# Optimization experiments

Measured on AMD Instinct MI355X. Metric: run time of the kernel, lower is better.

Reference implementation:

```python
import jax, jax.numpy as jnp
import numpy as np

N, X_DIM, Y_DIM, HID = 8192, 512, 2048 // 4, 2048
Y_DIM = 512

def setup_inputs() -> dict:
    key = jax.random.key(0)
    ks = jax.random.split(key, 10)
    def lin(k, fan_in, fan_out):
        lim = 1.0 / np.sqrt(fan_in)
        kw, kb = jax.random.split(k)
        W = jax.random.uniform(kw, (fan_in, fan_out), jnp.float32, -lim, lim)
        b = jax.random.uniform(kb, (fan_out,), jnp.float32, -lim, lim)
        return W, b
    mu_W1, mu_b1 = lin(ks[0], X_DIM, HID)
    mu_W2, mu_b2 = lin(ks[1], HID, Y_DIM)
    lv_W1, lv_b1 = lin(ks[2], X_DIM, HID)
    lv_W2, lv_b2 = lin(ks[3], HID, Y_DIM)
    return {
        "x_samples": jax.random.normal(ks[4], (N, X_DIM), jnp.float32),
        "y_samples": jax.random.normal(ks[5], (N, Y_DIM), jnp.float32),
        "mu_W1": mu_W1, "mu_b1": mu_b1, "mu_W2": mu_W2, "mu_b2": mu_b2,
        "lv_W1": lv_W1, "lv_b1": lv_b1, "lv_W2": lv_W2, "lv_b2": lv_b2,
    }

def reference(x_samples, y_samples, mu_W1, mu_b1, mu_W2, mu_b2, lv_W1, lv_b1, lv_W2, lv_b2):
    # MLP heads (GEMMs)
    mu = jax.nn.relu(x_samples @ mu_W1 + mu_b1) @ mu_W2 + mu_b2          # [N, D]
    logvar = jnp.tanh(jax.nn.relu(x_samples @ lv_W1 + lv_b1) @ lv_W2 + lv_b2)  # [N, D]
    w = 0.5 * jnp.exp(-logvar)                                           # 1/(2*exp(logvar))
    n = x_samples.shape[0]

    # positive: -mean_i sum_d (mu_id - y_id)^2 * w_id
    positive = -(((mu - y_samples) ** 2) * w).sum(axis=1).mean()

    # negative (exact decomposition of the [N,N,D] broadcast):
    # -(1/N^2) sum_{i,d} w_id * (N*mu_id^2 - 2*mu_id*Sy_d + Sy2_d)
    Sy = y_samples.sum(axis=0)          # [D]
    Sy2 = (y_samples ** 2).sum(axis=0)  # [D]
    negative = -(w * (n * mu ** 2 - 2.0 * mu * Sy + Sy2)).sum() / (n * n)

    return positive - negative
```

## Files before the change

kernel.cpp:

```cpp
#include <hip/hip_runtime.h>
#include <hip/hip_bf16.h>
#include <stdint.h>

#define NS   8192
#define XD   512
#define HD   2048
#define YD   512

typedef unsigned short u16;
using bf16x8 = __attribute__((ext_vector_type(8))) short;
using f32x4  = __attribute__((ext_vector_type(4))) float;

__device__ __forceinline__ float bf2f(u16 u) {
  union { uint32_t i; float f; } v; v.i = ((uint32_t)u) << 16; return v.f;
}
__device__ __forceinline__ u16 f2b(float f) {
  __hip_bfloat16 hb = __float2bfloat16(f);
  return *(const u16*)&hb;
}
__device__ __forceinline__ float ld_in(const void* p, int f32, size_t i) {
  return f32 ? ((const float*)p)[i] : bf2f(((const u16*)p)[i]);
}
#define GLDS(gp, lp) __builtin_amdgcn_global_load_lds( \
    (__attribute__((address_space(1))) void*)(gp),     \
    (__attribute__((address_space(3))) void*)(lp), 16, 0, 0)

__device__ __forceinline__ int probe_f32(const void* p, int n_u16, int* sflag) {
  if (threadIdx.x == 0) *sflag = 0;
  __syncthreads();
  const u16* q = (const u16*)p;
  int wild = 0;
  for (int i = threadIdx.x; i < n_u16; i += blockDim.x) {
    float v = bf2f(q[i]);
    if (!(fabsf(v) <= 1000.0f)) wild = 1;
  }
  if (wild) *sflag = 1;
  __syncthreads();
  int r = *sflag;
  __syncthreads();
  return r;
}

__global__ __launch_bounds__(256) void prep_all(
    const void* __restrict__ x,
    const void* w1m, const void* b1m, const void* w2m, const void* b2m,
    const void* w1l, const void* b1l, const void* w2l, const void* b2l,
    u16* __restrict__ xb, float* __restrict__ biasv,
    u16* __restrict__ W1t, u16* __restrict__ W2tm, u16* __restrict__ W2tl) {
  __shared__ u16 tile[64 * 72];
  __shared__ int sflag;
  const int b = blockIdx.x;
  const int tid = threadIdx.x;

  if (b < 2048) {
    if (!probe_f32(x, 1024, &sflag)) return;
    const size_t base = (size_t)b * 2048 + (size_t)tid * 8;
    alignas(16) u16 o[8];
    const float4* s = (const float4*)((const float*)x + base);
    float4 v0 = s[0], v1 = s[1];
    o[0]=f2b(v0.x); o[1]=f2b(v0.y); o[2]=f2b(v0.z); o[3]=f2b(v0.w);
    o[4]=f2b(v1.x); o[5]=f2b(v1.y); o[6]=f2b(v1.z); o[7]=f2b(v1.w);
    *(uint4*)(xb + base) = *(const uint4*)o;
  } else if (b == 2048) {
    const int f3 = probe_f32(b1m, 1024, &sflag);
    const int f5 = probe_f32(b2m, 512, &sflag);
    const int f7 = probe_f32(b1l, 1024, &sflag);
    const int f9 = probe_f32(b2l, 512, &sflag);
    for (int i = tid; i < 5120; i += 256) {
      float v;
      if (i < 2048)      v = ld_in(b1m, f3, i);
      else if (i < 4096) v = ld_in(b1l, f7, i - 2048);
      else if (i < 4608) v = ld_in(b2m, f5, i - 4096);
      else               v = ld_in(b2l, f9, i - 4608);
      biasv[i] = v;
    }
  } else {
    const int id = b - 2049, which = id >> 8, t = id & 255;
    const void* in; u16* out; int R, C;
    if (which == 0)      { in = w1m; out = W1t;                   R = XD; C = HD; }
    else if (which == 1) { in = w2m; out = W2tm;                  R = HD; C = YD; }
    else if (which == 2) { in = w1l; out = W1t + (size_t)HD * XD; R = XD; C = HD; }
    else                 { in = w2l; out = W2tl;                  R = HD; C = YD; }
    const int f = probe_f32(in, 1024, &sflag);
    const int nbx = C >> 6;
    const int c0 = (t % nbx) * 64, r0 = (t / nbx) * 64;
    const int r = tid >> 2, cc = (tid & 3) * 16;
    if (f) {
      const float4* s = (const float4*)((const float*)in + (size_t)(r0 + r) * C + c0 + cc);
#pragma unroll
      for (int k = 0; k < 4; ++k) {
        float4 v = s[k];
        tile[r * 72 + cc + k * 4 + 0] = f2b(v.x);
        tile[r * 72 + cc + k * 4 + 1] = f2b(v.y);
        tile[r * 72 + cc + k * 4 + 2] = f2b(v.z);
        tile[r * 72 + cc + k * 4 + 3] = f2b(v.w);
      }
    } else {
      const uint4* s = (const uint4*)((const u16*)in + (size_t)(r0 + r) * C + c0 + cc);
      *(uint4*)&tile[r * 72 + cc]     = s[0];
      *(uint4*)&tile[r * 72 + cc + 8] = s[1];
    }
    __syncthreads();
    const int i = tid >> 2, jc = (tid & 3) * 16;
    alignas(16) u16 o[16];
#pragma unroll
    for (int j = 0; j < 16; ++j) o[j] = tile[(jc + j) * 72 + i];
    uint4* dq = (uint4*)&out[(size_t)(c0 + i) * R + r0 + jc];
    dq[0] = ((const uint4*)o)[0];
    dq[1] = ((const uint4*)o)[1];
  }
}

__global__ __launch_bounds__(256) void gemm1_kernel(
    const void* __restrict__ xraw, const u16* __restrict__ xb,
    const void* __restrict__ y,
    const u16* __restrict__ W1t,
    const float* __restrict__ bias,
    float* __restrict__ Sy, float* __restrict__ Sy2,
    u16* __restrict__ h_mu, u16* __restrict__ h_lv) {
  constexpr int K = XD;
  __shared__ alignas(16) u16 As[128 * 64];
  __shared__ alignas(16) u16 Bs[128 * 64];
  __shared__ int sflag;

  const int tid = threadIdx.x;

  if (blockIdx.x < 64) {
    const int yf = probe_f32(y, 1024, &sflag);
    const int half = tid >> 7;
    const int c0 = (tid & 127) * 4;
    const int r0 = blockIdx.x * 128 + half * 64;
    float s0 = 0.f, s1 = 0.f, s2 = 0.f, s3 = 0.f;
    float q0 = 0.f, q1 = 0.f, q2 = 0.f, q3 = 0.f;
    for (int r = r0; r < r0 + 64; r += 4) {
#pragma unroll
      for (int rr = 0; rr < 4; ++rr) {
        float v0, v1, v2, v3;
        if (yf) {
          const float4 t4 = *(const float4*)((const float*)y + (size_t)(r + rr) * YD + c0);
          v0 = t4.x; v1 = t4.y; v2 = t4.z; v3 = t4.w;
        } else {
          const uint2 t2 = *(const uint2*)((const u16*)y + (size_t)(r + rr) * YD + c0);
          v0 = bf2f((u16)(t2.x & 0xffff)); v1 = bf2f((u16)(t2.x >> 16));
          v2 = bf2f((u16)(t2.y & 0xffff)); v3 = bf2f((u16)(t2.y >> 16));
        }
        s0 += v0; q0 += v0 * v0;  s1 += v1; q1 += v1 * v1;
        s2 += v2; q2 += v2 * v2;  s3 += v3; q3 += v3 * v3;
      }
    }
    atomicAdd(&Sy[c0],     s0);  atomicAdd(&Sy2[c0],     q0);
    atomicAdd(&Sy[c0 + 1], s1);  atomicAdd(&Sy2[c0 + 1], q1);
    atomicAdd(&Sy[c0 + 2], s2);  atomicAdd(&Sy2[c0 + 2], q2);
    atomicAdd(&Sy[c0 + 3], s3);  atomicAdd(&Sy2[c0 + 3], q3);
    return;
  }

  const u16* A = probe_f32(xraw, 1024, &sflag) ? xb : (const u16*)xraw;

  const int wid = tid >> 6, lane = tid & 63;
  const int id = blockIdx.x - 64;
  const int xcd = id & 7, slot = id >> 3;
  const int m_idx = slot & 7;
  const int n_idx = slot >> 3;
  const int bm0 = (xcd * 8 + m_idx) * 128;
  const int bn0 = n_idx * 128;

  const int mrow = (wid >> 1) * 64, ncol = (wid & 1) * 64;
  const int quad = lane >> 4, c16 = lane & 15, cswz = c16 & 7;
  const int srow = lane >> 3, sc = lane & 7;
  const int scg  = (sc ^ srow) * 8;

  f32x4 acc[4][4] = {};

  for (int k0 = 0; k0 < K; k0 += 64) {
#pragma unroll
    for (int j = 0; j < 4; ++j) {
      const int grp = wid * 4 + j, row = grp * 8 + srow;
      GLDS(A   + (size_t)(bm0 + row) * K + (k0 + scg), As + grp * 512);
      GLDS(W1t + (size_t)(bn0 + row) * K + (k0 + scg), Bs + grp * 512);
    }
    __syncthreads();
#pragma unroll
    for (int h = 0; h < 2; ++h) {
      const int off = ((h * 4 + quad) ^ cswz) * 8;
      bf16x8 af[4], bfr[4];
#pragma unroll
      for (int mi = 0; mi < 4; ++mi)
        af[mi] = *(const bf16x8*)&As[(mrow + mi * 16 + c16) * 64 + off];
#pragma unroll
      for (int ni = 0; ni < 4; ++ni)
        bfr[ni] = *(const bf16x8*)&Bs[(ncol + ni * 16 + c16) * 64 + off];
#pragma unroll
      for (int mi = 0; mi < 4; ++mi)
#pragma unroll
        for (int ni = 0; ni < 4; ++ni)
          acc[mi][ni] = __builtin_amdgcn_mfma_f32_16x16x32_bf16(
              af[mi], bfr[ni], acc[mi][ni], 0, 0, 0);
    }
    __syncthreads();
  }

  const bool is_lv = bn0 >= HD;
  u16* dst = is_lv ? h_lv : h_mu;
  const int cb = bn0 - (is_lv ? HD : 0);
#pragma unroll
  for (int ni = 0; ni < 4; ++ni) {
    const int gc = ncol + ni * 16 + c16;
    const float bv = bias[bn0 + gc];
#pragma unroll
    for (int mi = 0; mi < 4; ++mi)
#pragma unroll
      for (int r = 0; r < 4; ++r) {
        const int grow = bm0 + mrow + mi * 16 + quad * 4 + r;
        dst[(size_t)grow * HD + (cb + gc)] = f2b(fmaxf(acc[mi][ni][r] + bv, 0.f));
      }
  }
}

__global__ __launch_bounds__(256) void gemm2_dual(
    const u16* __restrict__ hm, const u16* __restrict__ hl,
    const u16* __restrict__ W2m, const u16* __restrict__ W2l,
    const float* __restrict__ b2m, const float* __restrict__ b2l,
    const void* __restrict__ y,
    const float* __restrict__ Sy, const float* __restrict__ Sy2,
    double* __restrict__ gacc, unsigned* __restrict__ counter,
    float* __restrict__ out) {
  constexpr int K = HD;
  __shared__ alignas(16) u16 Am[64 * 64];
  __shared__ alignas(16) u16 Al[64 * 64];
  __shared__ alignas(16) u16 Bm[128 * 64];
  __shared__ alignas(16) u16 Bl[128 * 64];
  __shared__ double bs[4];
  __shared__ int sflag;

  const int yf = probe_f32(y, 1024, &sflag);

  const int tid = threadIdx.x, wid = tid >> 6, lane = tid & 63;
  const int MT = NS / 64, NT = YD / 128;
  const int id = blockIdx.x;
  const int xcd = id & 7, slot = id >> 3;
  const int bm0 = (xcd * (MT >> 3) + slot / NT) * 64;
  const int bn0 = (slot % NT) * 128;

  const int mrow = (wid >> 1) * 32, ncol = (wid & 1) * 64;
  const int quad = lane >> 4, c16 = lane & 15, cswz = c16 & 7;
  const int srow = lane >> 3, sc = lane & 7;
  const int scg  = (sc ^ srow) * 8;

  f32x4 am[2][4] = {}, al[2][4] = {};

  for (int k0 = 0; k0 < K; k0 += 64) {
#pragma unroll
    for (int j = 0; j < 2; ++j) {
      const int grp = wid * 2 + j, row = grp * 8 + srow;
      const size_t go = (size_t)(bm0 + row) * K + (k0 + scg);
      GLDS(hm + go, Am + grp * 512);
      GLDS(hl + go, Al + grp * 512);
    }
#pragma unroll
    for (int j = 0; j < 4; ++j) {
      const int grp = wid * 4 + j, row = grp * 8 + srow;
      const size_t go = (size_t)(bn0 + row) * K + (k0 + scg);
      GLDS(W2m + go, Bm + grp * 512);
      GLDS(W2l + go, Bl + grp * 512);
    }
    __syncthreads();
#pragma unroll
    for (int h = 0; h < 2; ++h) {
      const int off = ((h * 4 + quad) ^ cswz) * 8;
      bf16x8 afm[2], afl[2], bfm[4], bfl[4];
#pragma unroll
      for (int mi = 0; mi < 2; ++mi) {
        const int rl = (mrow + mi * 16 + c16) * 64 + off;
        afm[mi] = *(const bf16x8*)&Am[rl];
        afl[mi] = *(const bf16x8*)&Al[rl];
      }
#pragma unroll
      for (int ni = 0; ni < 4; ++ni) {
        const int rl = (ncol + ni * 16 + c16) * 64 + off;
        bfm[ni] = *(const bf16x8*)&Bm[rl];
        bfl[ni] = *(const bf16x8*)&Bl[rl];
      }
#pragma unroll
      for (int mi = 0; mi < 2; ++mi)
#pragma unroll
        for (int ni = 0; ni < 4; ++ni) {
          am[mi][ni] = __builtin_amdgcn_mfma_f32_16x16x32_bf16(
              afm[mi], bfm[ni], am[mi][ni], 0, 0, 0);
          al[mi][ni] = __builtin_amdgcn_mfma_f32_16x16x32_bf16(
              afl[mi], bfl[ni], al[mi][ni], 0, 0, 0);
        }
    }
    __syncthreads();
  }

  const float invN = 1.0f / (float)NS;
  float s = 0.f;
#pragma unroll
  for (int ni = 0; ni < 4; ++ni) {
    const int gcol = bn0 + ncol + ni * 16 + c16;
    const float bmv = b2m[gcol], blv = b2l[gcol];
    const float syv = Sy[gcol], sy2v = Sy2[gcol];
#pragma unroll
    for (int mi = 0; mi < 2; ++mi)
#pragma unroll
      for (int r = 0; r < 4; ++r) {
        const int grow = bm0 + mrow + mi * 16 + quad * 4 + r;
        const float m   = am[mi][ni][r] + bmv;
        const float lvp = al[mi][ni][r] + blv;
        const float w   = 0.5f * expf(-tanhf(lvp));
        const float yv  = ld_in(y, yf, (size_t)grow * YD + gcol);
        s += w * (yv * yv - 2.f * m * yv + (2.f * m * syv - sy2v) * invN);
      }
  }
  for (int off = 32; off > 0; off >>= 1) s += __shfl_down(s, off);
  if (lane == 0) bs[wid] = (double)s;
  __syncthreads();
  if (tid == 0) {
    atomicAdd(gacc, bs[0] + bs[1] + bs[2] + bs[3]);
    __threadfence();
    const unsigned old = atomicAdd(counter, 1u);
    if (old == gridDim.x - 1) {
      const double g = atomicAdd(gacc, 0.0);
      out[0] = (float)(-g / (double)NS);
    }
  }
}

extern "C" void kernel_launch(void* const* d_in, const int* in_sizes, int n_in,
                              void* d_out, int out_size, void* d_ws, size_t ws_size,
                              hipStream_t stream) {
  char* ws = (char*)d_ws;
  double*   gacc    = (double*)ws;
  unsigned* counter = (unsigned*)(ws + 8);
  float*    Sy      = (float*)(ws + 128);
  float*    Sy2     = (float*)(ws + 2176);
  float*    biasv   = (float*)(ws + 4224);
  u16* xb   = (u16*)(ws + 24704);
  u16* W1t  = xb + (size_t)NS * XD;
  u16* W2tm = W1t + (size_t)2 * HD * XD;
  u16* W2tl = W2tm + (size_t)YD * HD;
  u16* h_mu = W2tl + (size_t)YD * HD;
  u16* h_lv = h_mu + (size_t)NS * HD;

  hipMemsetAsync(d_ws, 0, 4224, stream);

  prep_all<<<2049 + 1024, 256, 0, stream>>>(
      d_in[0], d_in[2], d_in[3], d_in[4], d_in[5],
      d_in[6], d_in[7], d_in[8], d_in[9],
      xb, biasv, W1t, W2tm, W2tl);

  const float* b1  = biasv;
  const float* b2m = biasv + 4096, *b2l = biasv + 4608;

  gemm1_kernel<<<64 + (NS / 128) * ((2 * HD) / 128), 256, 0, stream>>>(
      d_in[0], xb, d_in[1], W1t, b1, Sy, Sy2, h_mu, h_lv);

  gemm2_dual<<<(NS / 64) * (YD / 128), 256, 0, stream>>>(
      h_mu, h_lv, W2tm, W2tl, b2m, b2l, d_in[1], Sy, Sy2,
      gacc, counter, (float*)d_out);
}
```

Baseline: 232.0 us.

## Rewrite first GEMM as 256x256 double-buffered pipelined kernel with LDS-staged stores

The first-layer GEMM moves from 128x128 tiles with 4 waves to 256x256 tiles with 8 waves. It double-buffers the K-slices in LDS and interleaves async global-to-LDS loads with MFMA phases under explicit barriers, waitcnts and setprio. The output is staged through a swizzled LDS tile so global stores become coalesced 16-byte writes. The y column-sum reduction moves out of the GEMM launch into the prep kernel. Each block gets more data reuse and overlaps loads with compute, in exchange for 128KB of LDS per block and higher register pressure, which may limit occupancy.

```diff
diff --git a/kernel.cpp b/kernel.cpp
--- a/kernel.cpp
+++ b/kernel.cpp
@@ -45,8 +45,10 @@
     const void* __restrict__ x,
     const void* w1m, const void* b1m, const void* w2m, const void* b2m,
     const void* w1l, const void* b1l, const void* w2l, const void* b2l,
+    const void* __restrict__ y,
     u16* __restrict__ xb, float* __restrict__ biasv,
-    u16* __restrict__ W1t, u16* __restrict__ W2tm, u16* __restrict__ W2tl) {
+    u16* __restrict__ W1t, u16* __restrict__ W2tm, u16* __restrict__ W2tl,
+    float* __restrict__ Sy, float* __restrict__ Sy2) {
   __shared__ u16 tile[64 * 72];
   __shared__ int sflag;
   const int b = blockIdx.x;
@@ -74,7 +76,7 @@
       else               v = ld_in(b2l, f9, i - 4608);
       biasv[i] = v;
     }
-  } else {
+  } else if (b < 3073) {
     const int id = b - 2049, which = id >> 8, t = id & 255;
     const void* in; u16* out; int R, C;
     if (which == 0)      { in = w1m; out = W1t;                   R = XD; C = HD; }
@@ -108,28 +110,12 @@
     uint4* dq = (uint4*)&out[(size_t)(c0 + i) * R + r0 + jc];
     dq[0] = ((const uint4*)o)[0];
     dq[1] = ((const uint4*)o)[1];
-  }
-}
-
-__global__ __launch_bounds__(256) void gemm1_kernel(
-    const void* __restrict__ xraw, const u16* __restrict__ xb,
-    const void* __restrict__ y,
-    const u16* __restrict__ W1t,
-    const float* __restrict__ bias,
-    float* __restrict__ Sy, float* __restrict__ Sy2,
-    u16* __restrict__ h_mu, u16* __restrict__ h_lv) {
-  constexpr int K = XD;
-  __shared__ alignas(16) u16 As[128 * 64];
-  __shared__ alignas(16) u16 Bs[128 * 64];
-  __shared__ int sflag;
-
-  const int tid = threadIdx.x;
-
-  if (blockIdx.x < 64) {
+  } else {
+    const int id2 = b - 3073;
     const int yf = probe_f32(y, 1024, &sflag);
     const int half = tid >> 7;
     const int c0 = (tid & 127) * 4;
-    const int r0 = blockIdx.x * 128 + half * 64;
+    const int r0 = id2 * 128 + half * 64;
     float s0 = 0.f, s1 = 0.f, s2 = 0.f, s3 = 0.f;
     float q0 = 0.f, q1 = 0.f, q2 = 0.f, q3 = 0.f;
     for (int r = r0; r < r0 + 64; r += 4) {
@@ -152,70 +138,145 @@
     atomicAdd(&Sy[c0 + 1], s1);  atomicAdd(&Sy2[c0 + 1], q1);
     atomicAdd(&Sy[c0 + 2], s2);  atomicAdd(&Sy2[c0 + 2], q2);
     atomicAdd(&Sy[c0 + 3], s3);  atomicAdd(&Sy2[c0 + 3], q3);
-    return;
-  }
-
-  const u16* A = probe_f32(xraw, 1024, &sflag) ? xb : (const u16*)xraw;
+  }
+}
+
+#define SYNC_PRE do { \
+  __builtin_amdgcn_sched_barrier(0); \
+  __builtin_amdgcn_s_barrier(); \
+  asm volatile("s_waitcnt lgkmcnt(0)" ::: "memory"); \
+  __builtin_amdgcn_sched_barrier(0); \
+  __builtin_amdgcn_s_setprio(1); } while (0)
+#define SYNC_POST do { \
+  __builtin_amdgcn_s_setprio(0); \
+  __builtin_amdgcn_sched_barrier(0); \
+  __builtin_amdgcn_s_barrier(); \
+  __builtin_amdgcn_sched_barrier(0); } while (0)
+#define VMCNT4 asm volatile("s_waitcnt vmcnt(4)" ::: "memory")
+#define VMCNT0 asm volatile("s_waitcnt vmcnt(0)" ::: "memory")
+
+#define RD_A(MH, BUF) do { \
+  const u16* ab_ = &lds[((BUF)*2 + wm) * 8192]; \
+  _Pragma("unroll") for (int q_ = 0; q_ < 4; ++q_) \
+    _Pragma("unroll") for (int ks_ = 0; ks_ < 2; ++ks_) \
+      af[q_][ks_] = *(const bf16x8*)&ab_[((MH)*64 + q_*16 + c16)*64 + (((ks_*4+quad) ^ cswz) << 3)]; \
+} while (0)
+
+#define RD_B(NH, BUF) do { \
+  const u16* bb_ = &lds[32768 + ((BUF)*2 + (wn>>1)) * 8192]; \
+  _Pragma("unroll") for (int p_ = 0; p_ < 2; ++p_) \
+    _Pragma("unroll") for (int ks_ = 0; ks_ < 2; ++ks_) \
+      bf[(NH)*2+p_][ks_] = *(const bf16x8*)&bb_[((wn&1)*64 + ((NH)*2+p_)*16 + c16)*64 + (((ks_*4+quad) ^ cswz) << 3)]; \
+} while (0)
+
+#define MM(MH, NH) do { \
+  _Pragma("unroll") for (int ks_ = 0; ks_ < 2; ++ks_) \
+    _Pragma("unroll") for (int q_ = 0; q_ < 4; ++q_) \
+      _Pragma("unroll") for (int p_ = 0; p_ < 2; ++p_) \
+        acc[(MH)*4+q_][(NH)*2+p_] = __builtin_amdgcn_mfma_f32_16x16x32_bf16( \
+            af[q_][ks_], bf[(NH)*2+p_][ks_], acc[(MH)*4+q_][(NH)*2+p_], 0, 0, 0); \
+} while (0)
+
+#define ST_A(KT, HALF) do { if ((KT) < 8) { \
+  u16* lb_ = &lds[(((KT)&1)*2 + (HALF))*8192 + (wid << 9)]; \
+  const u16* sp_ = Aptr + (size_t)(bm0 + (HALF)*128 + (wid<<3) + srow)*512 + ((KT)<<6) + scg; \
+  GLDS(sp_, lb_); GLDS(sp_ + (size_t)64*512, lb_ + 4096); } } while (0)
+
+#define ST_B(KT, HALF) do { if ((KT) < 8) { \
+  u16* lb_ = &lds[32768 + (((KT)&1)*2 + (HALF))*8192 + (wid << 9)]; \
+  const u16* sp_ = W1t + (size_t)(bn0 + (HALF)*128 + (wid<<3) + srow)*512 + ((KT)<<6) + scg; \
+  GLDS(sp_, lb_); GLDS(sp_ + (size_t)64*512, lb_ + 4096); } } while (0)
+
+__global__ __launch_bounds__(512, 2) void gemm1_kernel(
+    const void* __restrict__ xraw, const u16* __restrict__ xb,
+    const u16* __restrict__ W1t,
+    const float* __restrict__ bias,
+    u16* __restrict__ h_mu, u16* __restrict__ h_lv) {
+  __shared__ alignas(16) u16 lds[65536];
+  __shared__ int sflag;
+  const int tid = threadIdx.x;
+
+  const u16* Aptr = probe_f32(xraw, 1024, &sflag) ? xb : (const u16*)xraw;
 
   const int wid = tid >> 6, lane = tid & 63;
-  const int id = blockIdx.x - 64;
+  const int wm = wid >> 2, wn = wid & 3;
+  const int quad = lane >> 4, c16 = lane & 15, cswz = c16 & 7;
+  const int srow = lane >> 3;
+  const int scg  = ((lane & 7) ^ srow) << 3;
+
+  const int id = blockIdx.x;
   const int xcd = id & 7, slot = id >> 3;
-  const int m_idx = slot & 7;
-  const int n_idx = slot >> 3;
-  const int bm0 = (xcd * 8 + m_idx) * 128;
-  const int bn0 = n_idx * 128;
-
-  const int mrow = (wid >> 1) * 64, ncol = (wid & 1) * 64;
-  const int quad = lane >> 4, c16 = lane & 15, cswz = c16 & 7;
-  const int srow = lane >> 3, sc = lane & 7;
-  const int scg  = (sc ^ srow) * 8;
-
-  f32x4 acc[4][4] = {};
-
-  for (int k0 = 0; k0 < K; k0 += 64) {
-#pragma unroll
-    for (int j = 0; j < 4; ++j) {
-      const int grp = wid * 4 + j, row = grp * 8 + srow;
-      GLDS(A   + (size_t)(bm0 + row) * K + (k0 + scg), As + grp * 512);
-      GLDS(W1t + (size_t)(bn0 + row) * K + (k0 + scg), Bs + grp * 512);
-    }
-    __syncthreads();
-#pragma unroll
-    for (int h = 0; h < 2; ++h) {
-      const int off = ((h * 4 + quad) ^ cswz) * 8;
-      bf16x8 af[4], bfr[4];
-#pragma unroll
-      for (int mi = 0; mi < 4; ++mi)
-        af[mi] = *(const bf16x8*)&As[(mrow + mi * 16 + c16) * 64 + off];
-#pragma unroll
-      for (int ni = 0; ni < 4; ++ni)
-        bfr[ni] = *(const bf16x8*)&Bs[(ncol + ni * 16 + c16) * 64 + off];
-#pragma unroll
-      for (int mi = 0; mi < 4; ++mi)
-#pragma unroll
-        for (int ni = 0; ni < 4; ++ni)
-          acc[mi][ni] = __builtin_amdgcn_mfma_f32_16x16x32_bf16(
-              af[mi], bfr[ni], acc[mi][ni], 0, 0, 0);
-    }
-    __syncthreads();
-  }
-
+  const int bm0 = (xcd * 4 + (slot & 3)) * 256;
+  const int bn0 = (slot >> 2) * 256;
+
+  f32x4 acc[8][4] = {};
+  bf16x8 af[4][2], bf[4][2];
+
+  ST_B(0, 0); ST_B(0, 1); ST_A(0, 0); ST_A(0, 1);
+  ST_B(1, 0); ST_B(1, 1);
+  VMCNT4;
+  __builtin_amdgcn_s_barrier();
+  __builtin_amdgcn_sched_barrier(0);
+
+#pragma unroll
+  for (int i = 0; i < 4; ++i) {
+    const int ka = 2 * i, kb = ka + 1;
+    const bool last = (i == 3);
+    RD_A(0, 0); RD_B(0, 0); ST_A(kb, 0);
+    SYNC_PRE; MM(0, 0); SYNC_POST;
+    RD_B(1, 0); ST_A(kb, 1);
+    SYNC_PRE; MM(0, 1); SYNC_POST;
+    RD_A(1, 0); ST_B(ka + 2, 0);
+    SYNC_PRE; MM(1, 0); SYNC_POST;
+    ST_B(ka + 2, 1);
+    SYNC_PRE; MM(1, 1);
+    if (!last) { VMCNT4; } else { VMCNT0; }
+    SYNC_POST;
+    RD_A(0, 1); RD_B(0, 1); ST_A(ka + 2, 0);
+    SYNC_PRE; MM(0, 0); SYNC_POST;
+    RD_B(1, 1); ST_A(ka + 2, 1);
+    SYNC_PRE; MM(0, 1); SYNC_POST;
+    RD_A(1, 1); ST_B(kb + 2, 0);
+    SYNC_PRE; MM(1, 0); SYNC_POST;
+    ST_B(kb + 2, 1);
+    SYNC_PRE; MM(1, 1);
+    if (!last) { VMCNT4; }
+    SYNC_POST;
+  }
+
+  u16* myl = &lds[wid * 8192];
   const bool is_lv = bn0 >= HD;
   u16* dst = is_lv ? h_lv : h_mu;
-  const int cb = bn0 - (is_lv ? HD : 0);
+  const int wncol = wn << 6;
+  const int gc0 = (bn0 - (is_lv ? HD : 0)) + wncol;
+  const int grow0 = bm0 + (wm << 7);
 #pragma unroll
   for (int ni = 0; ni < 4; ++ni) {
-    const int gc = ncol + ni * 16 + c16;
-    const float bv = bias[bn0 + gc];
-#pragma unroll
-    for (int mi = 0; mi < 4; ++mi)
+    const float bv = bias[bn0 + wncol + ni * 16 + c16];
+#pragma unroll
+    for (int mi = 0; mi < 8; ++mi)
 #pragma unroll
       for (int r = 0; r < 4; ++r) {
-        const int grow = bm0 + mrow + mi * 16 + quad * 4 + r;
-        dst[(size_t)grow * HD + (cb + gc)] = f2b(fmaxf(acc[mi][ni][r] + bv, 0.f));
-      }
-  }
-}
+        const int row = mi * 16 + (quad << 2) + r;
+        const int col = ni * 16 + c16;
+        myl[row * 64 + ((((col >> 3) ^ (row & 7)) << 3) | (col & 7))] =
+            f2b(fmaxf(acc[mi][ni][r] + bv, 0.f));
+      }
+  }
+#pragma unroll
+  for (int it = 0; it < 16; ++it) {
+    const int row = (it << 3) + (lane >> 3);
+    const int ch = lane & 7;
+    const uint4 v = *(const uint4*)&myl[row * 64 + ((ch ^ (row & 7)) << 3)];
+    *(uint4*)&dst[(size_t)(grow0 + row) * HD + gc0 + (ch << 3)] = v;
+  }
+}
+
+#undef RD_A
+#undef RD_B
+#undef MM
+#undef ST_A
+#undef ST_B
 
 __global__ __launch_bounds__(256) void gemm2_dual(
     const u16* __restrict__ hm, const u16* __restrict__ hl,
@@ -345,16 +406,16 @@
 
   hipMemsetAsync(d_ws, 0, 4224, stream);
 
-  prep_all<<<2049 + 1024, 256, 0, stream>>>(
+  prep_all<<<2049 + 1024 + 64, 256, 0, stream>>>(
       d_in[0], d_in[2], d_in[3], d_in[4], d_in[5],
-      d_in[6], d_in[7], d_in[8], d_in[9],
-      xb, biasv, W1t, W2tm, W2tl);
+      d_in[6], d_in[7], d_in[8], d_in[9], d_in[1],
+      xb, biasv, W1t, W2tm, W2tl, Sy, Sy2);
 
   const float* b1  = biasv;
   const float* b2m = biasv + 4096, *b2l = biasv + 4608;
 
-  gemm1_kernel<<<64 + (NS / 128) * ((2 * HD) / 128), 256, 0, stream>>>(
-      d_in[0], xb, d_in[1], W1t, b1, Sy, Sy2, h_mu, h_lv);
+  gemm1_kernel<<<(NS / 256) * ((2 * HD) / 256), 512, 0, stream>>>(
+      d_in[0], xb, W1t, b1, h_mu, h_lv);
 
   gemm2_dual<<<(NS / 64) * (YD / 128), 256, 0, stream>>>(
       h_mu, h_lv, W2tm, W2tl, b2m, b2l, d_in[1], Sy, Sy2,
```

Result: faster. 225.2 us (-2.9%).
